# Kernel tuning notes

Hardware: AMD Instinct MI355X
Metric: run time of the kernel (lower is better)

## Reference

```python
import jax, jax.numpy as jnp
import numpy as np

B, L, D, E, H = 8, 2048, 1024, 8, 2048


def setup_inputs() -> dict:
    key = jax.random.key(0)
    ks = jax.random.split(key, 5)
    scale_in = 1.0 / np.sqrt(D)
    scale_h = 1.0 / np.sqrt(H)
    return {
        "x": jax.random.normal(ks[0], (B, L, D), dtype=jnp.float32),
        "Wg": jax.random.normal(ks[1], (D, E), dtype=jnp.float32) * scale_in,
        "bg": jnp.zeros((E,), dtype=jnp.float32),
        "W1": jax.random.normal(ks[2], (E, D, H), dtype=jnp.float32) * scale_in,
        "b1": jnp.zeros((E, H), dtype=jnp.float32),
        "W2": jax.random.normal(ks[3], (E, H, D), dtype=jnp.float32) * scale_h,
        "b2": jnp.zeros((E, D), dtype=jnp.float32),
    }


def reference(x, Wg, bg, W1, b1, W2, b2):
    # x: [B, L, D] -> tokens [N, D]
    Bs, Ls, Ds = x.shape
    x_flat = x.reshape(-1, Ds)                                   # [N, D]
    gate_logits = x_flat @ Wg + bg                               # [N, E]
    gate_weights = jax.nn.softmax(gate_logits, axis=-1)          # [N, E]
    # top-1 gate (torch.topk with k=1)
    top_idx = jnp.argmax(gate_weights, axis=-1)                  # [N]
    top_w = jnp.max(gate_weights, axis=-1)                       # [N]
    # dense all-expert compute (matches torch.stack over experts)
    hidden = jax.nn.relu(jnp.einsum('nd,edh->neh', x_flat, W1) + b1)  # [N, E, H]
    expert_outputs = jnp.einsum('neh,ehd->ned', hidden, W2) + b2     # [N, E, D]
    # gather the selected expert per token, scale by its gate weight
    selected = jnp.take_along_axis(expert_outputs, top_idx[:, None, None], axis=1)[:, 0, :]  # [N, D]
    out_flat = top_w[:, None] * selected                          # [N, D]
    out = out_flat.reshape(Bs, Ls, Ds)
    return out, gate_weights
```

## Files before the change

kernel.cpp:

```cpp
#include <hip/hip_runtime.h>
#include <hip/hip_bf16.h>

#define N_TOK 16384
#define D_DIM 1024
#define E_NUM 8
#define H_DIM 2048
#define MT 32
#define FFN_BLK 512

typedef __attribute__((ext_vector_type(8))) short short8;
typedef __attribute__((ext_vector_type(4))) float floatx4;

__device__ __forceinline__ unsigned short f2bf_bits(float f) {
    __hip_bfloat16 h = __float2bfloat16(f);
    return *reinterpret_cast<unsigned short*>(&h);
}

__device__ __forceinline__ void async16(const void* g, void* l) {
    __builtin_amdgcn_global_load_lds(
        (const __attribute__((address_space(1))) unsigned int*)g,
        (__attribute__((address_space(3))) unsigned int*)l,
        16, 0, 0);
}

__global__ __launch_bounds__(256) void moe_gate_kernel(
    const float* __restrict__ x,
    const float* __restrict__ Wg,
    const float* __restrict__ bg,
    float* __restrict__ gw_out,
    float* __restrict__ topw,
    int* __restrict__ topidx,
    unsigned short* __restrict__ xb) {
    int wave = (blockIdx.x * blockDim.x + threadIdx.x) >> 6;
    int lane = threadIdx.x & 63;
    if (wave >= N_TOK) return;
    const float* xr = x + (size_t)wave * D_DIM;

    float4 xv[4];
#pragma unroll
    for (int i = 0; i < 4; i++)
        xv[i] = *(const float4*)(xr + i * 256 + lane * 4);

#pragma unroll
    for (int i = 0; i < 4; i++) {
        ushort4 o;
        o.x = f2bf_bits(xv[i].x); o.y = f2bf_bits(xv[i].y);
        o.z = f2bf_bits(xv[i].z); o.w = f2bf_bits(xv[i].w);
        *(ushort4*)(xb + (size_t)wave * D_DIM + i * 256 + lane * 4) = o;
    }

    float acc[8];
#pragma unroll
    for (int e = 0; e < 8; e++) acc[e] = 0.f;

#pragma unroll
    for (int i = 0; i < 4; i++) {
        const float xs4[4] = {xv[i].x, xv[i].y, xv[i].z, xv[i].w};
        const float* wp = Wg + ((size_t)(i * 256) + lane * 4) * 8;
#pragma unroll
        for (int j = 0; j < 4; j++) {
            float4 w0 = *(const float4*)(wp + j * 8);
            float4 w1 = *(const float4*)(wp + j * 8 + 4);
            float s = xs4[j];
            acc[0] += s * w0.x; acc[1] += s * w0.y;
            acc[2] += s * w0.z; acc[3] += s * w0.w;
            acc[4] += s * w1.x; acc[5] += s * w1.y;
            acc[6] += s * w1.z; acc[7] += s * w1.w;
        }
    }
#pragma unroll
    for (int e = 0; e < 8; e++) {
#pragma unroll
        for (int off = 32; off > 0; off >>= 1)
            acc[e] += __shfl_xor(acc[e], off, 64);
    }
#pragma unroll
    for (int e = 0; e < 8; e++) acc[e] += bg[e];

    float mx = acc[0]; int am = 0;
#pragma unroll
    for (int e = 1; e < 8; e++) { if (acc[e] > mx) { mx = acc[e]; am = e; } }
    float w[8], s = 0.f;
#pragma unroll
    for (int e = 0; e < 8; e++) { w[e] = expf(acc[e] - mx); s += w[e]; }
    float inv = 1.f / s;
#pragma unroll
    for (int e = 0; e < 8; e++) w[e] *= inv;

    if (lane == 0) {
        float4 a = make_float4(w[0], w[1], w[2], w[3]);
        float4 b = make_float4(w[4], w[5], w[6], w[7]);
        *(float4*)(gw_out + (size_t)wave * 8)     = a;
        *(float4*)(gw_out + (size_t)wave * 8 + 4) = b;
        topw[wave]   = w[am];
        topidx[wave] = am;
    }
}

__global__ __launch_bounds__(256) void moe_hist_scan_kernel(
    const int* __restrict__ topidx,
    int* __restrict__ offsets,
    int* __restrict__ cursor) {
    __shared__ int part[256][8];
    int tid = threadIdx.x;
    int c0 = 0, c1 = 0, c2 = 0, c3 = 0, c4 = 0, c5 = 0, c6 = 0, c7 = 0;
    for (int i = 0; i < N_TOK / 256; i++) {
        int idx = topidx[tid + (i << 8)];
        c0 += (idx == 0); c1 += (idx == 1); c2 += (idx == 2); c3 += (idx == 3);
        c4 += (idx == 4); c5 += (idx == 5); c6 += (idx == 6); c7 += (idx == 7);
    }
    part[tid][0] = c0; part[tid][1] = c1; part[tid][2] = c2; part[tid][3] = c3;
    part[tid][4] = c4; part[tid][5] = c5; part[tid][6] = c6; part[tid][7] = c7;
    __syncthreads();
    for (int s = 128; s > 0; s >>= 1) {
        if (tid < s) {
#pragma unroll
            for (int e = 0; e < 8; e++) part[tid][e] += part[tid + s][e];
        }
        __syncthreads();
    }
    if (tid == 0) {
        int run = 0;
        for (int e = 0; e < 8; e++) {
            offsets[e] = run;
            cursor[e]  = run;
            run += part[0][e];
        }
        offsets[8] = run;
    }
}

__global__ __launch_bounds__(256) void moe_scatter_kernel(
    const int* __restrict__ topidx,
    int* __restrict__ cursor,
    int* __restrict__ toksort) {
    __shared__ int lcnt[8];
    __shared__ int lbase[8];
    int tid = threadIdx.x;
    int t = blockIdx.x * blockDim.x + tid;
    if (tid < 8) lcnt[tid] = 0;
    __syncthreads();
    int e = topidx[t];
    int r = atomicAdd(&lcnt[e], 1);
    __syncthreads();
    if (tid < 8) lbase[tid] = atomicAdd(&cursor[tid], lcnt[tid]);
    __syncthreads();
    toksort[lbase[e] + r] = t;
}

__global__ __launch_bounds__(256) void transpose_cast_both(
    const float* __restrict__ W1, const float* __restrict__ W2,
    unsigned short* __restrict__ W1t, unsigned short* __restrict__ W2t) {
    __shared__ float tile[64][65];
    int id = blockIdx.x;
    const float* in; unsigned short* out; int R, C, cx, ry, e;
    if (id < 4096) {
        e = id >> 9; int t = id & 511;
        in = W1; out = W1t; R = 1024; C = 2048;
        cx = t & 31; ry = t >> 5;
    } else {
        id -= 4096;
        e = id >> 9; int t = id & 511;
        in = W2; out = W2t; R = 2048; C = 1024;
        cx = t & 15; ry = t >> 4;
    }
    const float* inE = in + (size_t)e * 2097152;
    unsigned short* outE = out + (size_t)e * 2097152;
    int c0 = cx << 6, r0 = ry << 6;
    int tr = threadIdx.x >> 4;
    int tc = (threadIdx.x & 15) << 2;
#pragma unroll
    for (int i = 0; i < 4; i++) {
        int r = tr + (i << 4);
        float4 v = *(const float4*)(inE + (size_t)(r0 + r) * C + c0 + tc);
        tile[r][tc + 0] = v.x; tile[r][tc + 1] = v.y;
        tile[r][tc + 2] = v.z; tile[r][tc + 3] = v.w;
    }
    __syncthreads();
#pragma unroll
    for (int it = 0; it < 2; it++) {
        int task = threadIdx.x + (it << 8);
        int c = task >> 3, rr = (task & 7) << 3;
        short8 o;
#pragma unroll
        for (int j = 0; j < 8; j++)
            ((unsigned short*)&o)[j] = f2bf_bits(tile[rr + j][c]);
        *(short8*)(outE + (size_t)(c0 + c) * R + r0 + rr) = o;
    }
}

__global__ __launch_bounds__(256) void gather_sorted_kernel(
    const unsigned short* __restrict__ xb, const int* __restrict__ toksort,
    unsigned short* __restrict__ xs) {
    int p = (blockIdx.x << 1) + (threadIdx.x >> 7);
    int tok = toksort[p];
    int c = (threadIdx.x & 127) << 3;
    float4 v = *(const float4*)(xb + (size_t)tok * D_DIM + c);
    *(float4*)(xs + (size_t)p * D_DIM + c) = v;
}

__device__ __forceinline__ int find_tile256(const int* offsets, int mt,
                                            int& row0, int& rows) {
    int cum = 0;
    for (int ee = 0; ee < E_NUM; ee++) {
        int o0 = offsets[ee], o1 = offsets[ee + 1];
        int tiles = (o1 - o0 + 255) >> 8;
        if (mt < cum + tiles) {
            row0 = o0 + ((mt - cum) << 8);
            rows = o1 - row0; if (rows > 256) rows = 256;
            return ee;
        }
        cum += tiles;
    }
    return -1;
}

#define MMQ(Q, NQ)                                                            \
    _Pragma("unroll") for (int mi = 0; mi < 4; mi++)                          \
    _Pragma("unroll") for (int ni = 0; ni < 2; ni++)                          \
    _Pragma("unroll") for (int kk = 0; kk < 2; kk++)                          \
        acc[(Q)*4 + mi][(NQ)*2 + ni] = __builtin_amdgcn_mfma_f32_16x16x32_bf16( \
            af[mi][kk], bf[ni][kk], acc[(Q)*4 + mi][(NQ)*2 + ni], 0, 0, 0);

#define VMC6 asm volatile("s_waitcnt vmcnt(6)" ::: "memory")
#define VMC8 asm volatile("s_waitcnt vmcnt(8)" ::: "memory")
#define VMNO ((void)0)

#define PHASE(RDS, STG, Q, NQ, VM)                                            \
    RDS;                                                                      \
    STG;                                                                      \
    __builtin_amdgcn_sched_barrier(0);                                        \
    __builtin_amdgcn_s_barrier();                                             \
    asm volatile("s_waitcnt lgkmcnt(0)" ::: "memory");                        \
    __builtin_amdgcn_sched_barrier(0);                                        \
    __builtin_amdgcn_s_setprio(1);                                            \
    MMQ(Q, NQ);                                                               \
    __builtin_amdgcn_s_setprio(0);                                            \
    VM;                                                                       \
    __builtin_amdgcn_s_barrier();                                             \
    __builtin_amdgcn_sched_barrier(0);

template<int LDK>
__device__ __forceinline__ void gemm256_kloop(
    const unsigned short* __restrict__ Ag,
    const unsigned short* __restrict__ Bg,
    int row0, int n0, int ntiles,
    unsigned short* LDSU, floatx4 (&acc)[8][4]) {

    const int tid = threadIdx.x;
    const int l = tid & 63, w = tid >> 6;
    const int lq = l >> 4, lrow = l & 15, l3 = l >> 3;
    const int wm = w & 1, wn = w >> 1;
    const int kc = ((l & 7) ^ (l3 & 7)) << 3;
    const int gx = l & 7;

    const unsigned short* pA[2][2];
    const unsigned short* pB[2][2];
#pragma unroll
    for (int j = 0; j < 2; j++) {
        int s = w * 16 + j * 8 + l3;
#pragma unroll
        for (int h = 0; h < 2; h++) {
            int rA = (s & 63) + h * 64 + ((s >> 6) & 1) * 128;
            int pr = row0 + rA; if (pr > N_TOK - 1) pr = N_TOK - 1;
            pA[j][h] = Ag + (size_t)pr * LDK + kc;
            int cB = (s & 31) + h * 32 + (s >> 5) * 64;
            pB[j][h] = Bg + (size_t)(n0 + cB) * LDK + kc;
        }
    }
    unsigned short* ldsA = LDSU;
    unsigned short* ldsB = LDSU + 32768;
    const int wslot = w * 1024;

    auto STA = [&](int buf, int half, int t) {
        async16(pA[0][half] + ((size_t)t << 6),
                ldsA + buf * 16384 + half * 8192 + wslot);
        async16(pA[1][half] + ((size_t)t << 6),
                ldsA + buf * 16384 + half * 8192 + wslot + 512);
    };
    auto STB = [&](int buf, int half, int t) {
        async16(pB[0][half] + ((size_t)t << 6),
                ldsB + buf * 16384 + half * 8192 + wslot);
        async16(pB[1][half] + ((size_t)t << 6),
                ldsB + buf * 16384 + half * 8192 + wslot + 512);
    };

    short8 af[4][2], bf[2][2];
    const int asb = wm * 64 + lrow;
    const int bsb = wn * 32 + lrow;
    auto RA = [&](int buf, int q) {
        const unsigned short* Ab = ldsA + buf * 16384 + q * 8192;
#pragma unroll
        for (int mi = 0; mi < 4; mi++) {
            int slot = asb + mi * 16;
#pragma unroll
            for (int kk = 0; kk < 2; kk++) {
                int g = (kk * 4 + lq) ^ gx;
                af[mi][kk] = *(const short8*)(Ab + slot * 64 + g * 8);
            }
        }
    };
    auto RB = [&](int buf, int nq) {
        const unsigned short* Bb = ldsB + buf * 16384 + nq * 8192;
#pragma unroll
        for (int ni = 0; ni < 2; ni++) {
            int slot = bsb + ni * 16;
#pragma unroll
            for (int kk = 0; kk < 2; kk++) {
                int g = (kk * 4 + lq) ^ gx;
                bf[ni][kk] = *(const short8*)(Bb + slot * 64 + g * 8);
            }
        }
    };

    STA(0, 0, 0); STB(0, 0, 0); STA(0, 1, 0); STB(0, 1, 0);
    STA(1, 0, 1); STB(1, 0, 1);
    VMC8;
    __builtin_amdgcn_s_barrier();
    __builtin_amdgcn_sched_barrier(0);

    const int NT2 = ntiles >> 1;
    for (int i = 0; i < NT2; i++) {
        const int t1 = 2 * i + 1;
        int t2 = 2 * i + 2; if (t2 > ntiles - 1) t2 = ntiles - 1;
        int t3 = 2 * i + 3; if (t3 > ntiles - 1) t3 = ntiles - 1;
        PHASE((RA(0, 0), RB(0, 0)), STA(1, 1, t1), 0, 0, VMC6);
        PHASE((RB(0, 1)),           STB(1, 1, t1), 0, 1, VMNO);
        PHASE((RA(0, 1), RB(0, 0)), STA(0, 0, t2), 1, 0, VMNO);
        PHASE((RB(0, 1)),           STB(0, 0, t2), 1, 1, VMC8);
        PHASE((RA(1, 0), RB(1, 0)), STA(0, 1, t2), 0, 0, VMC6);
        PHASE((RB(1, 1)),           STB(0, 1, t2), 0, 1, VMNO);
        PHASE((RA(1, 1), RB(1, 0)), STA(1, 0, t3), 1, 0, VMNO);
        PHASE((RB(1, 1)),           STB(1, 0, t3), 1, 1, VMC8);
    }
    asm volatile("s_waitcnt vmcnt(0)" ::: "memory");
    __syncthreads();
}

__global__ __launch_bounds__(512, 2) void moe_ffn1_256(
    const unsigned short* __restrict__ xs,
    const unsigned short* __restrict__ W1t,
    const float* __restrict__ b1,
    const int* __restrict__ offsets,
    unsigned short* __restrict__ hb) {

    __shared__ __align__(16) unsigned short LDSU[65536];

    int nwgx = gridDim.x;
    int nwg = nwgx * gridDim.y;
    int id = blockIdx.y * nwgx + blockIdx.x;
    int q8 = nwg >> 3, r8 = nwg & 7;
    int xcd = id & 7, rank = id >> 3;
    int swz = (xcd < r8 ? xcd * (q8 + 1) : r8 * (q8 + 1) + (xcd - r8) * q8) + rank;
    int bx = swz % nwgx, by = swz / nwgx;

    int row0, rows;
    int e = find_tile256(offsets, bx, row0, rows);
    if (e < 0) return;
    int n0 = by << 8;

    const unsigned short* Be = W1t + (size_t)e * H_DIM * D_DIM;

    floatx4 acc[8][4];
#pragma unroll
    for (int mi = 0; mi < 8; mi++)
#pragma unroll
        for (int ni = 0; ni < 4; ni++) acc[mi][ni] = floatx4{0.f, 0.f, 0.f, 0.f};

    gemm256_kloop<D_DIM>(xs, Be, row0, n0, D_DIM / 64, LDSU, acc);

    const int tid = threadIdx.x;
    const int l = tid & 63, w = tid >> 6;
    const int lq = l >> 4, lrow = l & 15;
    const int wm = w & 1, wn = w >> 1;

    float bias[4];
#pragma unroll
    for (int ni = 0; ni < 4; ni++)
        bias[ni] = b1[e * H_DIM + n0 + wn * 64 + ni * 16 + lrow];

#pragma unroll
    for (int mi = 0; mi < 8; mi++) {
#pragma unroll
        for (int ni = 0; ni < 4; ni++) {
#pragma unroll
            for (int rr = 0; rr < 4; rr++) {
                int rl = wm * 128 + mi * 16 + lq * 4 + rr;
                int cl = wn * 64 + ni * 16 + lrow;
                float v = acc[mi][ni][rr] + bias[ni];
                v = v > 0.f ? v : 0.f;
                LDSU[rl * 256 + cl] = f2bf_bits(v);
            }
        }
    }
    __syncthreads();
    int trow = tid >> 1, tcol = (tid & 1) << 7;
    if (trow < rows) {
        unsigned short* dst = hb + (size_t)(row0 + trow) * H_DIM + n0 + tcol;
        const unsigned short* src = LDSU + trow * 256 + tcol;
#pragma unroll
        for (int i2 = 0; i2 < 16; i2++)
            *(short8*)(dst + i2 * 8) = *(const short8*)(src + i2 * 8);
    }
}

__global__ __launch_bounds__(512, 2) void moe_ffn2_256(
    const unsigned short* __restrict__ hb,
    const unsigned short* __restrict__ W2t,
    const float* __restrict__ b2,
    const int* __restrict__ offsets,
    const int* __restrict__ toksort,
    const float* __restrict__ topw,
    float* __restrict__ out) {

    __shared__ __align__(16) unsigned short LDSU[65536];

    int nwgx = gridDim.x;
    int nwg = nwgx * gridDim.y;
    int id = blockIdx.y * nwgx + blockIdx.x;
    int q8 = nwg >> 3, r8 = nwg & 7;
    int xcd = id & 7, rank = id >> 3;
    int swz = (xcd < r8 ? xcd * (q8 + 1) : r8 * (q8 + 1) + (xcd - r8) * q8) + rank;
    int bx = swz % nwgx, by = swz / nwgx;

    int row0, rows;
    int e = find_tile256(offsets, bx, row0, rows);
    if (e < 0) return;
    int n0 = by << 8;

    const unsigned short* Be = W2t + (size_t)e * D_DIM * H_DIM;

    floatx4 acc[8][4];
#pragma unroll
    for (int mi = 0; mi < 8; mi++)
#pragma unroll
        for (int ni = 0; ni < 4; ni++) acc[mi][ni] = floatx4{0.f, 0.f, 0.f, 0.f};

    gemm256_kloop<H_DIM>(hb, Be, row0, n0, H_DIM / 64, LDSU, acc);

    const int tid = threadIdx.x;
    const int l = tid & 63, w = tid >> 6;
    const int lq = l >> 4, lrow = l & 15;
    const int wm = w & 1, wn = w >> 1;

    float bias[4];
#pragma unroll
    for (int ni = 0; ni < 4; ni++)
        bias[ni] = b2[e * D_DIM + n0 + wn * 64 + ni * 16 + lrow];

    float* LDSF = (float*)LDSU;
#pragma unroll
    for (int h = 0; h < 2; h++) {
        __syncthreads();
        if (wm == h) {
#pragma unroll
            for (int mi = 0; mi < 8; mi++) {
#pragma unroll
                for (int ni = 0; ni < 4; ni++) {
#pragma unroll
                    for (int rr = 0; rr < 4; rr++) {
                        int rl = mi * 16 + lq * 4 + rr;
                        int cl = wn * 64 + ni * 16 + lrow;
                        LDSF[rl * 256 + cl] = acc[mi][ni][rr] + bias[ni];
                    }
                }
            }
        }
        __syncthreads();
        int rloc = tid >> 2, seg = (tid & 3) << 6;
        int rl = h * 128 + rloc;
        if (rl < rows) {
            int p = row0 + rl;
            int tok = toksort[p];
            float tw = topw[tok];
            float* dst = out + (size_t)tok * D_DIM + n0 + seg;
            const float* src = LDSF + rloc * 256 + seg;
#pragma unroll
            for (int i2 = 0; i2 < 16; i2++) {
                float4 v = *(const float4*)(src + i2 * 4);
                v.x *= tw; v.y *= tw; v.z *= tw; v.w *= tw;
                *(float4*)(dst + i2 * 4) = v;
            }
        }
    }
}

__global__ __launch_bounds__(FFN_BLK, 2) void moe_ffn_kernel(
    const float* __restrict__ x,
    const float* __restrict__ W1, const float* __restrict__ b1,
    const float* __restrict__ W2, const float* __restrict__ b2,
    const int* __restrict__ offsets,
    const int* __restrict__ toksort,
    const float* __restrict__ topw,
    float* __restrict__ out) {

    __shared__ __align__(16) unsigned short h1c[MT * 1024];
    float* xs = (float*)h1c;

    int bid = blockIdx.x;
    int e = -1, row0 = 0, rows = 0, cum = 0;
    for (int ee = 0; ee < E_NUM; ee++) {
        int o0 = offsets[ee], o1 = offsets[ee + 1];
        int tiles = (o1 - o0 + MT - 1) / MT;
        if (bid < cum + tiles) {
            e = ee;
            row0 = o0 + (bid - cum) * MT;
            rows = (o1 - row0 < MT) ? (o1 - row0) : MT;
            break;
        }
        cum += tiles;
    }
    if (e < 0) return;

    int tid = threadIdx.x;
    const float* W1e = W1 + (size_t)e * D_DIM * H_DIM;
    const float* W2e = W2 + (size_t)e * H_DIM * D_DIM;

    int m_st = tid >> 4;
    int j_st = tid & 15;
    int m_cl = (m_st < rows) ? m_st : (rows - 1);
    int tok_st = toksort[row0 + m_cl];

    float acc2x[MT], acc2y[MT];
#pragma unroll
    for (int m = 0; m < MT; m++) { acc2x[m] = 0.f; acc2y[m] = 0.f; }

    int d0 = tid * 2;

    for (int half = 0; half < 2; half++) {
        int ha = half * 1024 + tid;
        int hb_ = ha + 512;

        float a1a[MT], a1b[MT];
#pragma unroll
        for (int m = 0; m < MT; m++) { a1a[m] = 0.f; a1b[m] = 0.f; }

        for (int dc = 0; dc < 8; dc++) {
            __syncthreads();
            {
                const float4* src =
                    (const float4*)(x + (size_t)tok_st * D_DIM + dc * 128 + j_st * 8);
                float4 v0 = src[0], v1 = src[1];
                float4* dst = (float4*)(xs + m_st * 128 + j_st * 8);
                dst[0] = v0; dst[1] = v1;
            }
            __syncthreads();
            const float* w1pa = W1e + (size_t)(dc * 128) * H_DIM + ha;
            const float* w1pb = W1e + (size_t)(dc * 128) * H_DIM + hb_;
            for (int d2 = 0; d2 < 64; d2++) {
                float wa0 = w1pa[0], wa1 = w1pa[H_DIM];
                float wb0 = w1pb[0], wb1 = w1pb[H_DIM];
                w1pa += 2 * H_DIM; w1pb += 2 * H_DIM;
#pragma unroll
                for (int m = 0; m < MT; m++) {
                    float2 xv = *(const float2*)(xs + m * 128 + d2 * 2);
                    a1a[m] += xv.x * wa0; a1a[m] += xv.y * wa1;
                    a1b[m] += xv.x * wb0; a1b[m] += xv.y * wb1;
                }
            }
        }

        float bba = b1[e * H_DIM + ha];
        float bbb = b1[e * H_DIM + hb_];
        __syncthreads();
#pragma unroll
        for (int m = 0; m < MT; m++) {
            float va = a1a[m] + bba; va = va > 0.f ? va : 0.f;
            float vb = a1b[m] + bbb; vb = vb > 0.f ? vb : 0.f;
            h1c[m * 1024 + tid]       = f2bf_bits(va);
            h1c[m * 1024 + 512 + tid] = f2bf_bits(vb);
        }
        __syncthreads();

        const float* w2p = W2e + (size_t)(half * 1024) * D_DIM + d0;
        for (int hh = 0; hh < 1024; hh += 2) {
            float2 w2a = *(const float2*)(w2p);
            float2 w2b = *(const float2*)(w2p + D_DIM);
            w2p += 2 * D_DIM;
#pragma unroll
            for (int m = 0; m < MT; m++) {
                unsigned int u = *(const unsigned int*)(h1c + m * 1024 + hh);
                float h0  = __uint_as_float(u << 16);
                float h1v = __uint_as_float(u & 0xffff0000u);
                acc2x[m] += h0 * w2a.x; acc2x[m] += h1v * w2b.x;
                acc2y[m] += h0 * w2a.y; acc2y[m] += h1v * w2b.y;
            }
        }
    }

    float bb0 = b2[e * D_DIM + d0];
    float bb1 = b2[e * D_DIM + d0 + 1];
#pragma unroll
    for (int m = 0; m < MT; m++) {
        if (m < rows) {
            int tok  = toksort[row0 + m];
            float tw = topw[tok];
            float2 o;
            o.x = tw * (acc2x[m] + bb0);
            o.y = tw * (acc2y[m] + bb1);
            *(float2*)(out + (size_t)tok * D_DIM + d0) = o;
        }
    }
}

extern "C" void kernel_launch(void* const* d_in, const int* in_sizes, int n_in,
                              void* d_out, int out_size, void* d_ws, size_t ws_size,
                              hipStream_t stream) {
    const float* x  = (const float*)d_in[0];
    const float* Wg = (const float*)d_in[1];
    const float* bg = (const float*)d_in[2];
    const float* W1 = (const float*)d_in[3];
    const float* b1 = (const float*)d_in[4];
    const float* W2 = (const float*)d_in[5];
    const float* b2 = (const float*)d_in[6];

    float* out = (float*)d_out;
    float* gw  = out + (size_t)N_TOK * D_DIM;

    char* ws = (char*)d_ws;
    int*   counts  = (int*)ws;
    int*   cursor  = counts + 8;
    int*   offsets = cursor + 8;
    int*   topidx  = (int*)(ws + 128);
    float* topw    = (float*)(ws + 128 + 4 * (size_t)N_TOK);
    int*   toksort = (int*)(ws + 128 + 8 * (size_t)N_TOK);

    const size_t off_xs  = 256ull << 10;
    const size_t off_w1t = off_xs  + (32ull << 20);
    const size_t off_w2t = off_w1t + (32ull << 20);
    const size_t off_hb  = off_w2t + (32ull << 20);
    const size_t off_xb  = off_hb;
    const size_t need    = off_hb  + (64ull << 20);

    if (ws_size >= need) {
        unsigned short* xs  = (unsigned short*)(ws + off_xs);
        unsigned short* W1t = (unsigned short*)(ws + off_w1t);
        unsigned short* W2t = (unsigned short*)(ws + off_w2t);
        unsigned short* hb  = (unsigned short*)(ws + off_hb);
        unsigned short* xb  = (unsigned short*)(ws + off_xb);

        moe_gate_kernel<<<N_TOK / 4, 256, 0, stream>>>(
            x, Wg, bg, gw, topw, topidx, xb);
        moe_hist_scan_kernel<<<1, 256, 0, stream>>>(topidx, offsets, cursor);
        moe_scatter_kernel<<<N_TOK / 256, 256, 0, stream>>>(topidx, cursor, toksort);

        transpose_cast_both<<<8192, 256, 0, stream>>>(W1, W2, W1t, W2t);
        gather_sorted_kernel<<<N_TOK / 2, 256, 0, stream>>>(xb, toksort, xs);

        moe_ffn1_256<<<dim3(N_TOK / 256 + E_NUM, H_DIM / 256), 512, 0, stream>>>(
            xs, W1t, b1, offsets, hb);
        moe_ffn2_256<<<dim3(N_TOK / 256 + E_NUM, D_DIM / 256), 512, 0, stream>>>(
            hb, W2t, b2, offsets, toksort, topw, out);
    } else {
        unsigned short* xb = (unsigned short*)(ws + (256ull << 10));
        moe_gate_kernel<<<N_TOK / 4, 256, 0, stream>>>(
            x, Wg, bg, gw, topw, topidx, xb);
        moe_hist_scan_kernel<<<1, 256, 0, stream>>>(topidx, offsets, cursor);
        moe_scatter_kernel<<<N_TOK / 256, 256, 0, stream>>>(topidx, cursor, toksort);
        moe_ffn_kernel<<<N_TOK / MT + E_NUM, FFN_BLK, 0, stream>>>(
            x, W1, b1, W2, b2, offsets, toksort, topw, out);
    }
}
```

Measured before the change: 552.0 us.

## Fuse FFN stages into persistent ticket-scheduled kernel and merge prep kernels

Merges the weight transpose-cast into the gate kernel launch and folds the bf16 cast and gather of x into the scatter kernel, dropping the xb intermediate and two launches. The two grouped GEMM stages become one persistent kernel of 256 blocks that pull tiles from an atomic ticket. FFN2 tiles spin-wait on per-M-tile completion counters, so the second GEMM of one tile can overlap the first GEMM of others and the inter-kernel drain disappears. This adds spin-wait and atomic overhead and risks stalls if ordering or occupancy assumptions fail. The 64-token gather loop also has less parallelism per block.

```diff
diff --git a/kernel.cpp b/kernel.cpp
--- a/kernel.cpp
+++ b/kernel.cpp
@@ -7,6 +7,9 @@
 #define H_DIM 2048
 #define MT 32
 #define FFN_BLK 512
+#define MTILES 72
+#define T1_TASKS (MTILES * 8)
+#define T2_TASKS (MTILES * 4)
 
 typedef __attribute__((ext_vector_type(8))) short short8;
 typedef __attribute__((ext_vector_type(4))) float floatx4;
@@ -23,15 +26,61 @@
         16, 0, 0);
 }
 
-__global__ __launch_bounds__(256) void moe_gate_kernel(
+__global__ __launch_bounds__(256) void moe_gate_transpose_fused(
     const float* __restrict__ x,
     const float* __restrict__ Wg,
     const float* __restrict__ bg,
     float* __restrict__ gw_out,
     float* __restrict__ topw,
     int* __restrict__ topidx,
-    unsigned short* __restrict__ xb) {
-    int wave = (blockIdx.x * blockDim.x + threadIdx.x) >> 6;
+    const float* __restrict__ W1,
+    const float* __restrict__ W2,
+    unsigned short* __restrict__ W1t,
+    unsigned short* __restrict__ W2t) {
+
+    __shared__ float tile[64][65];
+
+    if (blockIdx.x < 8192) {
+        int id = blockIdx.x;
+        const float* in; unsigned short* out; int R, C, cx, ry, e;
+        if (id < 4096) {
+            e = id >> 9; int t = id & 511;
+            in = W1; out = W1t; R = 1024; C = 2048;
+            cx = t & 31; ry = t >> 5;
+        } else {
+            id -= 4096;
+            e = id >> 9; int t = id & 511;
+            in = W2; out = W2t; R = 2048; C = 1024;
+            cx = t & 15; ry = t >> 4;
+        }
+        const float* inE = in + (size_t)e * 2097152;
+        unsigned short* outE = out + (size_t)e * 2097152;
+        int c0 = cx << 6, r0 = ry << 6;
+        int tr = threadIdx.x >> 4;
+        int tc = (threadIdx.x & 15) << 2;
+#pragma unroll
+        for (int i = 0; i < 4; i++) {
+            int r = tr + (i << 4);
+            float4 v = *(const float4*)(inE + (size_t)(r0 + r) * C + c0 + tc);
+            tile[r][tc + 0] = v.x; tile[r][tc + 1] = v.y;
+            tile[r][tc + 2] = v.z; tile[r][tc + 3] = v.w;
+        }
+        __syncthreads();
+#pragma unroll
+        for (int it = 0; it < 2; it++) {
+            int task = threadIdx.x + (it << 8);
+            int c = task >> 3, rr = (task & 7) << 3;
+            short8 o;
+#pragma unroll
+            for (int j = 0; j < 8; j++)
+                ((unsigned short*)&o)[j] = f2bf_bits(tile[rr + j][c]);
+            *(short8*)(outE + (size_t)(c0 + c) * R + r0 + rr) = o;
+        }
+        return;
+    }
+
+    int bid = blockIdx.x - 8192;
+    int wave = ((bid << 8) + threadIdx.x) >> 6;
     int lane = threadIdx.x & 63;
     if (wave >= N_TOK) return;
     const float* xr = x + (size_t)wave * D_DIM;
@@ -40,14 +89,6 @@
 #pragma unroll
     for (int i = 0; i < 4; i++)
         xv[i] = *(const float4*)(xr + i * 256 + lane * 4);
-
-#pragma unroll
-    for (int i = 0; i < 4; i++) {
-        ushort4 o;
-        o.x = f2bf_bits(xv[i].x); o.y = f2bf_bits(xv[i].y);
-        o.z = f2bf_bits(xv[i].z); o.w = f2bf_bits(xv[i].w);
-        *(ushort4*)(xb + (size_t)wave * D_DIM + i * 256 + lane * 4) = o;
-    }
 
     float acc[8];
 #pragma unroll
@@ -97,12 +138,81 @@
     }
 }
 
+__global__ __launch_bounds__(256) void moe_gate_kernel(
+    const float* __restrict__ x,
+    const float* __restrict__ Wg,
+    const float* __restrict__ bg,
+    float* __restrict__ gw_out,
+    float* __restrict__ topw,
+    int* __restrict__ topidx) {
+    int wave = (blockIdx.x * blockDim.x + threadIdx.x) >> 6;
+    int lane = threadIdx.x & 63;
+    if (wave >= N_TOK) return;
+    const float* xr = x + (size_t)wave * D_DIM;
+
+    float4 xv[4];
+#pragma unroll
+    for (int i = 0; i < 4; i++)
+        xv[i] = *(const float4*)(xr + i * 256 + lane * 4);
+
+    float acc[8];
+#pragma unroll
+    for (int e = 0; e < 8; e++) acc[e] = 0.f;
+#pragma unroll
+    for (int i = 0; i < 4; i++) {
+        const float xs4[4] = {xv[i].x, xv[i].y, xv[i].z, xv[i].w};
+        const float* wp = Wg + ((size_t)(i * 256) + lane * 4) * 8;
+#pragma unroll
+        for (int j = 0; j < 4; j++) {
+            float4 w0 = *(const float4*)(wp + j * 8);
+            float4 w1 = *(const float4*)(wp + j * 8 + 4);
+            float s = xs4[j];
+            acc[0] += s * w0.x; acc[1] += s * w0.y;
+            acc[2] += s * w0.z; acc[3] += s * w0.w;
+            acc[4] += s * w1.x; acc[5] += s * w1.y;
+            acc[6] += s * w1.z; acc[7] += s * w1.w;
+        }
+    }
+#pragma unroll
+    for (int e = 0; e < 8; e++) {
+#pragma unroll
+        for (int off = 32; off > 0; off >>= 1)
+            acc[e] += __shfl_xor(acc[e], off, 64);
+    }
+#pragma unroll
+    for (int e = 0; e < 8; e++) acc[e] += bg[e];
+
+    float mx = acc[0]; int am = 0;
+#pragma unroll
+    for (int e = 1; e < 8; e++) { if (acc[e] > mx) { mx = acc[e]; am = e; } }
+    float w[8], s = 0.f;
+#pragma unroll
+    for (int e = 0; e < 8; e++) { w[e] = expf(acc[e] - mx); s += w[e]; }
+    float inv = 1.f / s;
+#pragma unroll
+    for (int e = 0; e < 8; e++) w[e] *= inv;
+
+    if (lane == 0) {
+        float4 a = make_float4(w[0], w[1], w[2], w[3]);
+        float4 b = make_float4(w[4], w[5], w[6], w[7]);
+        *(float4*)(gw_out + (size_t)wave * 8)     = a;
+        *(float4*)(gw_out + (size_t)wave * 8 + 4) = b;
+        topw[wave]   = w[am];
+        topidx[wave] = am;
+    }
+}
+
 __global__ __launch_bounds__(256) void moe_hist_scan_kernel(
     const int* __restrict__ topidx,
     int* __restrict__ offsets,
-    int* __restrict__ cursor) {
+    int* __restrict__ cursor,
+    int* __restrict__ ctrl) {
     __shared__ int part[256][8];
     int tid = threadIdx.x;
+    if (ctrl) {
+        if (tid == 72) ctrl[0] = 0;
+        else if (tid < 72) ctrl[8 + tid] = 0;
+    }
     int c0 = 0, c1 = 0, c2 = 0, c3 = 0, c4 = 0, c5 = 0, c6 = 0, c7 = 0;
     for (int i = 0; i < N_TOK / 256; i++) {
         int idx = topidx[tid + (i << 8)];
@@ -127,6 +237,44 @@
             run += part[0][e];
         }
         offsets[8] = run;
+    }
+}
+
+__global__ __launch_bounds__(256) void moe_scatter_gather(
+    const float* __restrict__ x,
+    const int* __restrict__ topidx,
+    int* __restrict__ cursor,
+    int* __restrict__ toksort,
+    unsigned short* __restrict__ xs) {
+    __shared__ int lcnt[8];
+    __shared__ int lbase[8];
+    __shared__ int s_pos[64];
+    int tid = threadIdx.x;
+    int base = blockIdx.x << 6;
+    if (tid < 8) lcnt[tid] = 0;
+    __syncthreads();
+    int e = 0, r = 0;
+    if (tid < 64) {
+        e = topidx[base + tid];
+        r = atomicAdd(&lcnt[e], 1);
+    }
+    __syncthreads();
+    if (tid < 8) lbase[tid] = atomicAdd(&cursor[tid], lcnt[tid]);
+    __syncthreads();
+    if (tid < 64) {
+        int p = lbase[e] + r;
+        toksort[p] = base + tid;
+        s_pos[tid] = p;
+    }
+    __syncthreads();
+    for (int rr = 0; rr < 64; rr++) {
+        int tok = base + rr;
+        int p = s_pos[rr];
+        float4 v = *(const float4*)(x + (size_t)tok * D_DIM + (tid << 2));
+        ushort4 o;
+        o.x = f2bf_bits(v.x); o.y = f2bf_bits(v.y);
+        o.z = f2bf_bits(v.z); o.w = f2bf_bits(v.w);
+        *(ushort4*)(xs + (size_t)p * D_DIM + (tid << 2)) = o;
     }
 }
 
@@ -146,57 +294,6 @@
     if (tid < 8) lbase[tid] = atomicAdd(&cursor[tid], lcnt[tid]);
     __syncthreads();
     toksort[lbase[e] + r] = t;
-}
-
-__global__ __launch_bounds__(256) void transpose_cast_both(
-    const float* __restrict__ W1, const float* __restrict__ W2,
-    unsigned short* __restrict__ W1t, unsigned short* __restrict__ W2t) {
-    __shared__ float tile[64][65];
-    int id = blockIdx.x;
-    const float* in; unsigned short* out; int R, C, cx, ry, e;
-    if (id < 4096) {
-        e = id >> 9; int t = id & 511;
-        in = W1; out = W1t; R = 1024; C = 2048;
-        cx = t & 31; ry = t >> 5;
-    } else {
-        id -= 4096;
-        e = id >> 9; int t = id & 511;
-        in = W2; out = W2t; R = 2048; C = 1024;
-        cx = t & 15; ry = t >> 4;
-    }
-    const float* inE = in + (size_t)e * 2097152;
-    unsigned short* outE = out + (size_t)e * 2097152;
-    int c0 = cx << 6, r0 = ry << 6;
-    int tr = threadIdx.x >> 4;
-    int tc = (threadIdx.x & 15) << 2;
-#pragma unroll
-    for (int i = 0; i < 4; i++) {
-        int r = tr + (i << 4);
-        float4 v = *(const float4*)(inE + (size_t)(r0 + r) * C + c0 + tc);
-        tile[r][tc + 0] = v.x; tile[r][tc + 1] = v.y;
-        tile[r][tc + 2] = v.z; tile[r][tc + 3] = v.w;
-    }
-    __syncthreads();
-#pragma unroll
-    for (int it = 0; it < 2; it++) {
-        int task = threadIdx.x + (it << 8);
-        int c = task >> 3, rr = (task & 7) << 3;
-        short8 o;
-#pragma unroll
-        for (int j = 0; j < 8; j++)
-            ((unsigned short*)&o)[j] = f2bf_bits(tile[rr + j][c]);
-        *(short8*)(outE + (size_t)(c0 + c) * R + r0 + rr) = o;
-    }
-}
-
-__global__ __launch_bounds__(256) void gather_sorted_kernel(
-    const unsigned short* __restrict__ xb, const int* __restrict__ toksort,
-    unsigned short* __restrict__ xs) {
-    int p = (blockIdx.x << 1) + (threadIdx.x >> 7);
-    int tok = toksort[p];
-    int c = (threadIdx.x & 127) << 3;
-    float4 v = *(const float4*)(xb + (size_t)tok * D_DIM + c);
-    *(float4*)(xs + (size_t)p * D_DIM + c) = v;
 }
 
 __device__ __forceinline__ int find_tile256(const int* offsets, int mt,
@@ -337,149 +434,151 @@
     __syncthreads();
 }
 
-__global__ __launch_bounds__(512, 2) void moe_ffn1_256(
+__global__ __launch_bounds__(512, 2) void moe_ffn_fused(
     const unsigned short* __restrict__ xs,
     const unsigned short* __restrict__ W1t,
     const float* __restrict__ b1,
-    const int* __restrict__ offsets,
-    unsigned short* __restrict__ hb) {
-
-    __shared__ __align__(16) unsigned short LDSU[65536];
-
-    int nwgx = gridDim.x;
-    int nwg = nwgx * gridDim.y;
-    int id = blockIdx.y * nwgx + blockIdx.x;
-    int q8 = nwg >> 3, r8 = nwg & 7;
-    int xcd = id & 7, rank = id >> 3;
-    int swz = (xcd < r8 ? xcd * (q8 + 1) : r8 * (q8 + 1) + (xcd - r8) * q8) + rank;
-    int bx = swz % nwgx, by = swz / nwgx;
-
-    int row0, rows;
-    int e = find_tile256(offsets, bx, row0, rows);
-    if (e < 0) return;
-    int n0 = by << 8;
-
-    const unsigned short* Be = W1t + (size_t)e * H_DIM * D_DIM;
-
-    floatx4 acc[8][4];
-#pragma unroll
-    for (int mi = 0; mi < 8; mi++)
-#pragma unroll
-        for (int ni = 0; ni < 4; ni++) acc[mi][ni] = floatx4{0.f, 0.f, 0.f, 0.f};
-
-    gemm256_kloop<D_DIM>(xs, Be, row0, n0, D_DIM / 64, LDSU, acc);
-
-    const int tid = threadIdx.x;
-    const int l = tid & 63, w = tid >> 6;
-    const int lq = l >> 4, lrow = l & 15;
-    const int wm = w & 1, wn = w >> 1;
-
-    float bias[4];
-#pragma unroll
-    for (int ni = 0; ni < 4; ni++)
-        bias[ni] = b1[e * H_DIM + n0 + wn * 64 + ni * 16 + lrow];
-
-#pragma unroll
-    for (int mi = 0; mi < 8; mi++) {
-#pragma unroll
-        for (int ni = 0; ni < 4; ni++) {
-#pragma unroll
-            for (int rr = 0; rr < 4; rr++) {
-                int rl = wm * 128 + mi * 16 + lq * 4 + rr;
-                int cl = wn * 64 + ni * 16 + lrow;
-                float v = acc[mi][ni][rr] + bias[ni];
-                v = v > 0.f ? v : 0.f;
-                LDSU[rl * 256 + cl] = f2bf_bits(v);
-            }
-        }
-    }
-    __syncthreads();
-    int trow = tid >> 1, tcol = (tid & 1) << 7;
-    if (trow < rows) {
-        unsigned short* dst = hb + (size_t)(row0 + trow) * H_DIM + n0 + tcol;
-        const unsigned short* src = LDSU + trow * 256 + tcol;
-#pragma unroll
-        for (int i2 = 0; i2 < 16; i2++)
-            *(short8*)(dst + i2 * 8) = *(const short8*)(src + i2 * 8);
-    }
-}
-
-__global__ __launch_bounds__(512, 2) void moe_ffn2_256(
-    const unsigned short* __restrict__ hb,
+    unsigned short* __restrict__ hb,
     const unsigned short* __restrict__ W2t,
     const float* __restrict__ b2,
     const int* __restrict__ offsets,
     const int* __restrict__ toksort,
     const float* __restrict__ topw,
-    float* __restrict__ out) {
+    float* __restrict__ out,
+    int* __restrict__ ctrl) {
 
     __shared__ __align__(16) unsigned short LDSU[65536];
-
-    int nwgx = gridDim.x;
-    int nwg = nwgx * gridDim.y;
-    int id = blockIdx.y * nwgx + blockIdx.x;
-    int q8 = nwg >> 3, r8 = nwg & 7;
-    int xcd = id & 7, rank = id >> 3;
-    int swz = (xcd < r8 ? xcd * (q8 + 1) : r8 * (q8 + 1) + (xcd - r8) * q8) + rank;
-    int bx = swz % nwgx, by = swz / nwgx;
-
-    int row0, rows;
-    int e = find_tile256(offsets, bx, row0, rows);
-    if (e < 0) return;
-    int n0 = by << 8;
-
-    const unsigned short* Be = W2t + (size_t)e * D_DIM * H_DIM;
-
-    floatx4 acc[8][4];
-#pragma unroll
-    for (int mi = 0; mi < 8; mi++)
-#pragma unroll
-        for (int ni = 0; ni < 4; ni++) acc[mi][ni] = floatx4{0.f, 0.f, 0.f, 0.f};
-
-    gemm256_kloop<H_DIM>(hb, Be, row0, n0, H_DIM / 64, LDSU, acc);
+    __shared__ int s_task;
 
     const int tid = threadIdx.x;
     const int l = tid & 63, w = tid >> 6;
     const int lq = l >> 4, lrow = l & 15;
     const int wm = w & 1, wn = w >> 1;
-
-    float bias[4];
-#pragma unroll
-    for (int ni = 0; ni < 4; ni++)
-        bias[ni] = b2[e * D_DIM + n0 + wn * 64 + ni * 16 + lrow];
-
-    float* LDSF = (float*)LDSU;
-#pragma unroll
-    for (int h = 0; h < 2; h++) {
+    int* ticket = ctrl;
+    int* done   = ctrl + 8;
+
+    for (;;) {
         __syncthreads();
-        if (wm == h) {
-#pragma unroll
-            for (int mi = 0; mi < 8; mi++) {
-#pragma unroll
-                for (int ni = 0; ni < 4; ni++) {
-#pragma unroll
-                    for (int rr = 0; rr < 4; rr++) {
-                        int rl = mi * 16 + lq * 4 + rr;
-                        int cl = wn * 64 + ni * 16 + lrow;
-                        LDSF[rl * 256 + cl] = acc[mi][ni][rr] + bias[ni];
+        if (tid == 0) s_task = atomicAdd(ticket, 1);
+        __syncthreads();
+        const int task = s_task;
+        if (task >= T1_TASKS + T2_TASKS) break;
+
+        if (task < T1_TASKS) {
+            const int mt = task >> 3, ht = task & 7;
+            int row0, rows;
+            const int e = find_tile256(offsets, mt, row0, rows);
+            if (e >= 0) {
+                const int n0 = ht << 8;
+                floatx4 acc[8][4];
+#pragma unroll
+                for (int mi = 0; mi < 8; mi++)
+#pragma unroll
+                    for (int ni = 0; ni < 4; ni++)
+                        acc[mi][ni] = floatx4{0.f, 0.f, 0.f, 0.f};
+
+                gemm256_kloop<D_DIM>(xs, W1t + (size_t)e * H_DIM * D_DIM,
+                                     row0, n0, D_DIM / 64, LDSU, acc);
+
+                float bias[4];
+#pragma unroll
+                for (int ni = 0; ni < 4; ni++)
+                    bias[ni] = b1[e * H_DIM + n0 + wn * 64 + ni * 16 + lrow];
+#pragma unroll
+                for (int mi = 0; mi < 8; mi++) {
+#pragma unroll
+                    for (int ni = 0; ni < 4; ni++) {
+#pragma unroll
+                        for (int rr = 0; rr < 4; rr++) {
+                            int rl = wm * 128 + mi * 16 + lq * 4 + rr;
+                            int cl = wn * 64 + ni * 16 + lrow;
+                            float v = acc[mi][ni][rr] + bias[ni];
+                            v = v > 0.f ? v : 0.f;
+                            LDSU[rl * 256 + cl] = f2bf_bits(v);
+                        }
                     }
                 }
+                __syncthreads();
+                int trow = tid >> 1, tcol = (tid & 1) << 7;
+                if (trow < rows) {
+                    unsigned short* dst =
+                        hb + (size_t)(row0 + trow) * H_DIM + n0 + tcol;
+                    const unsigned short* src = LDSU + trow * 256 + tcol;
+#pragma unroll
+                    for (int i2 = 0; i2 < 16; i2++)
+                        *(short8*)(dst + i2 * 8) = *(const short8*)(src + i2 * 8);
+                }
             }
-        }
-        __syncthreads();
-        int rloc = tid >> 2, seg = (tid & 3) << 6;
-        int rl = h * 128 + rloc;
-        if (rl < rows) {
-            int p = row0 + rl;
-            int tok = toksort[p];
-            float tw = topw[tok];
-            float* dst = out + (size_t)tok * D_DIM + n0 + seg;
-            const float* src = LDSF + rloc * 256 + seg;
-#pragma unroll
-            for (int i2 = 0; i2 < 16; i2++) {
-                float4 v = *(const float4*)(src + i2 * 4);
-                v.x *= tw; v.y *= tw; v.z *= tw; v.w *= tw;
-                *(float4*)(dst + i2 * 4) = v;
+            __threadfence();
+            __syncthreads();
+            if (tid == 0)
+                __hip_atomic_fetch_add(&done[mt], 1, __ATOMIC_RELEASE,
+                                       __HIP_MEMORY_SCOPE_AGENT);
+        } else {
+            const int t2 = task - T1_TASKS;
+            const int mt = t2 >> 2, dt = t2 & 3;
+            int row0, rows;
+            const int e = find_tile256(offsets, mt, row0, rows);
+            if (e >= 0) {
+                if (tid == 0) {
+                    int sp = 0;
+                    while (__hip_atomic_load(&done[mt], __ATOMIC_ACQUIRE,
+                                             __HIP_MEMORY_SCOPE_AGENT) < 8) {
+                        if (++sp > 100000000) break;
+                    }
+                }
+                __syncthreads();
+                const int n0 = dt << 8;
+                floatx4 acc[8][4];
+#pragma unroll
+                for (int mi = 0; mi < 8; mi++)
+#pragma unroll
+                    for (int ni = 0; ni < 4; ni++)
+                        acc[mi][ni] = floatx4{0.f, 0.f, 0.f, 0.f};
+
+                gemm256_kloop<H_DIM>(hb, W2t + (size_t)e * D_DIM * H_DIM,
+                                     row0, n0, H_DIM / 64, LDSU, acc);
+
+                float bias[4];
+#pragma unroll
+                for (int ni = 0; ni < 4; ni++)
+                    bias[ni] = b2[e * D_DIM + n0 + wn * 64 + ni * 16 + lrow];
+
+                float* LDSF = (float*)LDSU;
+#pragma unroll
+                for (int h = 0; h < 2; h++) {
+                    __syncthreads();
+                    if (wm == h) {
+#pragma unroll
+                        for (int mi = 0; mi < 8; mi++) {
+#pragma unroll
+                            for (int ni = 0; ni < 4; ni++) {
+#pragma unroll
+                                for (int rr = 0; rr < 4; rr++) {
+                                    int rl = mi * 16 + lq * 4 + rr;
+                                    int cl = wn * 64 + ni * 16 + lrow;
+                                    LDSF[rl * 256 + cl] = acc[mi][ni][rr] + bias[ni];
+                                }
+                            }
+                        }
+                    }
+                    __syncthreads();
+                    int rloc = tid >> 2, seg = (tid & 3) << 6;
+                    int rl = h * 128 + rloc;
+                    if (rl < rows) {
+                        int p = row0 + rl;
+                        int tok = toksort[p];
+                        float tw = topw[tok];
+                        float* dst = out + (size_t)tok * D_DIM + n0 + seg;
+                        const float* src = LDSF + rloc * 256 + seg;
+#pragma unroll
+                        for (int i2 = 0; i2 < 16; i2++) {
+                            float4 v = *(const float4*)(src + i2 * 4);
+                            v.x *= tw; v.y *= tw; v.z *= tw; v.w *= tw;
+                            *(float4*)(dst + i2 * 4) = v;
+                        }
+                    }
+                }
             }
         }
     }
@@ -624,12 +723,12 @@
     int*   topidx  = (int*)(ws + 128);
     float* topw    = (float*)(ws + 128 + 4 * (size_t)N_TOK);
     int*   toksort = (int*)(ws + 128 + 8 * (size_t)N_TOK);
+    int*   ctrl    = (int*)(ws + (200ull << 10));
 
     const size_t off_xs  = 256ull << 10;
     const size_t off_w1t = off_xs  + (32ull << 20);
     const size_t off_w2t = off_w1t + (32ull << 20);
     const size_t off_hb  = off_w2t + (32ull << 20);
-    const size_t off_xb  = off_hb;
     const size_t need    = off_hb  + (64ull << 20);
 
     if (ws_size >= need) {
@@ -637,25 +736,19 @@
         unsigned short* W1t = (unsigned short*)(ws + off_w1t);
         unsigned short* W2t = (unsigned short*)(ws + off_w2t);
         unsigned short* hb  = (unsigned short*)(ws + off_hb);
-        unsigned short* xb  = (unsigned short*)(ws + off_xb);
-
+
+        moe_gate_transpose_fused<<<12288, 256, 0, stream>>>(
+            x, Wg, bg, gw, topw, topidx, W1, W2, W1t, W2t);
+        moe_hist_scan_kernel<<<1, 256, 0, stream>>>(topidx, offsets, cursor, ctrl);
+        moe_scatter_gather<<<N_TOK / 64, 256, 0, stream>>>(
+            x, topidx, cursor, toksort, xs);
+        moe_ffn_fused<<<256, 512, 0, stream>>>(
+            xs, W1t, b1, hb, W2t, b2, offsets, toksort, topw, out, ctrl);
+    } else {
         moe_gate_kernel<<<N_TOK / 4, 256, 0, stream>>>(
-            x, Wg, bg, gw, topw, topidx, xb);
-        moe_hist_scan_kernel<<<1, 256, 0, stream>>>(topidx, offsets, cursor);
-        moe_scatter_kernel<<<N_TOK / 256, 256, 0, stream>>>(topidx, cursor, toksort);
-
-        transpose_cast_both<<<8192, 256, 0, stream>>>(W1, W2, W1t, W2t);
-        gather_sorted_kernel<<<N_TOK / 2, 256, 0, stream>>>(xb, toksort, xs);
-
-        moe_ffn1_256<<<dim3(N_TOK / 256 + E_NUM, H_DIM / 256), 512, 0, stream>>>(
-            xs, W1t, b1, offsets, hb);
-        moe_ffn2_256<<<dim3(N_TOK / 256 + E_NUM, D_DIM / 256), 512, 0, stream>>>(
-            hb, W2t, b2, offsets, toksort, topw, out);
-    } else {
-        unsigned short* xb = (unsigned short*)(ws + (256ull << 10));
-        moe_gate_kernel<<<N_TOK / 4, 256, 0, stream>>>(
-            x, Wg, bg, gw, topw, topidx, xb);
-        moe_hist_scan_kernel<<<1, 256, 0, stream>>>(topidx, offsets, cursor);
+            x, Wg, bg, gw, topw, topidx);
+        moe_hist_scan_kernel<<<1, 256, 0, stream>>>(topidx, offsets, cursor,
+                                                    (int*)nullptr);
         moe_scatter_kernel<<<N_TOK / 256, 256, 0, stream>>>(topidx, cursor, toksort);
         moe_ffn_kernel<<<N_TOK / MT + E_NUM, FFN_BLK, 0, stream>>>(
             x, W1, b1, W2, b2, offsets, toksort, topw, out);
```

Result: slower. 753.8 us (+36.5%).
